# Optimization experiments

Measured on AMD Instinct MI355X. Metric: run time of the kernel, lower is better.

Reference implementation:

```python
import jax, jax.numpy as jnp
import numpy as np

SR = 22050.0  # samplerate; nyquist = SR/2


def _conv1d(x, w, b, pad):
    # x: [B, Cin, T], w: [Cout, Cin, K]
    y = jax.lax.conv_general_dilated(x, w, (1,), [(pad, pad)],
                                     dimension_numbers=('NCH', 'OIH', 'NCH'))
    return y + b[None, :, None]


def _lrelu(x):
    return jnp.where(x >= 0, x, 0.2 * x)


def _lin_upsample(x, factor):
    # torch F.upsample(mode='linear', align_corners=False) ~ half-pixel linear resize
    B, C, T = x.shape
    return jax.image.resize(x, (B, C, T * factor), method='linear')


def _oscillator_bank(f, a, sr):
    # f, a: [B, n_osc, T] -> audio [B, T]
    f = jnp.clip(f, 20.0, sr / 2.0)
    phase = jnp.cumsum(f * (2.0 * np.pi / sr), axis=-1)  # cumulative phase integration
    return jnp.sum(jnp.sin(phase) * a, axis=1)


def _noise_bank2(mags, noise):
    # mags: [B, n_coeffs, n_frames] rfft magnitudes per frame; noise: [B, total_samples]
    B, n_coeffs, n_frames = mags.shape
    window = (n_coeffs - 1) * 2
    hop = window // 2
    total = hop * n_frames
    padded = jnp.pad(noise, ((0, 0), (0, hop)))           # [B, total + hop]
    blocks = padded.reshape(B, n_frames + 1, hop)
    frames = jnp.concatenate([blocks[:, :-1], blocks[:, 1:]], axis=-1)  # [B, n_frames, window]
    spec = jnp.fft.rfft(frames, axis=-1)                   # [B, n_frames, n_coeffs]
    spec = spec * mags.transpose(0, 2, 1)                  # filter white noise per frame
    filt = jnp.fft.irfft(spec, n=window, axis=-1)          # (torch normalized rfft/irfft scales cancel)
    out = jnp.zeros((B, hop * (n_frames + 1)), filt.dtype)
    out = out.at[:, :n_frames * hop].add(filt[..., :hop].reshape(B, -1))
    out = out.at[:, hop:].add(filt[..., hop:].reshape(B, -1))
    return out[:, :total].reshape(B, 1, total)


def _forward(x, noise, mw0, mb0, mw1, mb1, mw2, mb2, mw3, mb3, fw, fb,
             gw0, gb0, gw1, gb1, gw2, gb2, gw3, gb3, lw, lb,
             nw0, nb0, nw1, nb1, nw2, nb2, nw3, nb3, nlw, nlb):
    B, _, T = x.shape
    up = noise.shape[1] // T  # upsample_factor = output_size // input_size
    n_osc = fw.shape[0]

    # oscillator frequency ranges (constants, as in __init__)
    stops = np.geomspace(20.0, SR / 2.0, num=n_osc)
    diffs = np.diff(np.concatenate([[0.0], stops]))
    starts = jnp.asarray(stops - diffs, jnp.float32)[None, :, None]
    diffs_j = jnp.asarray(diffs, jnp.float32)[None, :, None]

    # loudness path (main2 -> loudness ** 2)
    h = x
    for w_, b_ in ((gw0, gb0), (gw1, gb1), (gw2, gb2), (gw3, gb3)):
        h = _lrelu(_conv1d(h, w_, b_, 1))
    loud = _conv1d(h, lw, lb, 1) ** 2  # [B, n_osc, T]

    # frequency path (main -> sigmoid -> map to [start, stop])
    h = x
    for w_, b_ in ((mw0, mb0), (mw1, mb1), (mw2, mb2), (mw3, mb3)):
        h = _lrelu(_conv1d(h, w_, b_, 1))
    f = starts + jax.nn.sigmoid(_conv1d(h, fw, fb, 1)) * diffs_j  # [B, n_osc, T]

    h = x
    for w_, b_ in ((nw0, nb0), (nw1, nb1), (nw2, nb2), (nw3, nb3)):
        h = jnp.repeat(h, 2, axis=-1)
        h = _lrelu(_conv1d(h, w_, b_, 3))
    n_l = _conv1d(h, nlw, nlb, 1) ** 2  # [B, 17, 1024]

    loud = _lin_upsample(loud, up)  # [B, n_osc, output_size]
    f = _lin_upsample(f, up)
    harmonic = _oscillator_bank(f, loud, SR).reshape(B, 1, -1)
    return harmonic + _noise_bank2(n_l, noise)


def setup_inputs() -> dict:
    key = jax.random.key(0)
    ks = jax.random.split(key, 40)
    B, Cin, T, c, n_osc, out_size = 16, 128, 64, 512, 128, 16384
    n_coeffs = out_size // 1024 + 1  # 17
    inp = {}
    inp['x'] = jax.random.normal(ks[0], (B, Cin, T), jnp.float32)
    inp['noise'] = jax.random.uniform(ks[1], (B, out_size), jnp.float32, minval=-1.0, maxval=1.0)
    specs = [('mw0', c, Cin, 3), ('mw1', c, c, 3), ('mw2', c, c, 3), ('mw3', c, c, 3), ('fw', n_osc, c, 3),
             ('gw0', c, Cin, 3), ('gw1', c, c, 3), ('gw2', c, c, 3), ('gw3', c, c, 3), ('lw', n_osc, c, 3),
             ('nw0', c, Cin, 7), ('nw1', c, c, 7), ('nw2', c, c, 7), ('nw3', c, c, 7), ('nlw', n_coeffs, c, 3)]
    for j, (nm, o, i, ksz) in enumerate(specs):
        kw, kb = jax.random.split(ks[2 + j])
        inp[nm] = jax.random.normal(kw, (o, i, ksz), jnp.float32) * (1.0 / np.sqrt(i * ksz))
        inp[nm.replace('w', 'b', 1)] = jax.random.normal(kb, (o,), jnp.float32) * 0.01
    return inp


def reference(x, noise, mw0, mb0, mw1, mb1, mw2, mb2, mw3, mb3, fw, fb,
              gw0, gb0, gw1, gb1, gw2, gb2, gw3, gb3, lw, lb,
              nw0, nb0, nw1, nb1, nw2, nb2, nw3, nb3, nlw, nlb):
    return _forward(x, noise, mw0, mb0, mw1, mb1, mw2, mb2, mw3, mb3, fw, fb,
                    gw0, gb0, gw1, gb1, gw2, gb2, gw3, gb3, lw, lb,
                    nw0, nb0, nw1, nb1, nw2, nb2, nw3, nb3, nlw, nlb)
```

## Files before the change

kernel.cpp:

```cpp
#include <hip/hip_runtime.h>
#include <math.h>

#define ACT_LRELU  0
#define ACT_SIGMAP 1
#define ACT_SQUARE 2

typedef __attribute__((ext_vector_type(8))) short v8s;
typedef __attribute__((ext_vector_type(4))) short v4s;
typedef __attribute__((ext_vector_type(16))) float f32x16;

static __device__ __forceinline__ float lrelu(float x) { return x >= 0.f ? x : 0.2f * x; }

static __device__ __forceinline__ short bf16rne(float x) {
  unsigned u = __float_as_uint(x);
  unsigned r = (u + 0x7FFFu + ((u >> 16) & 1u)) >> 16;
  return (short)r;
}
static __device__ __forceinline__ float bf16tof(short h) {
  return __uint_as_float(((unsigned)(unsigned short)h) << 16);
}
static __device__ __forceinline__ void split3(float v, short& h, short& l, short& q) {
  h = bf16rne(v); float r1 = v - bf16tof(h);
  l = bf16rne(r1); float r2 = r1 - bf16tof(l);
  q = bf16rne(r2);
}

__global__ void __launch_bounds__(256) prep_mg(
    const float* __restrict__ x, short* __restrict__ xm3,
    const float* mw0, const float* mw1, const float* mw2, const float* mw3, const float* fw,
    const float* gw0, const float* gw1, const float* gw2, const float* gw3, const float* lw,
    short* __restrict__ mP, short* __restrict__ gP)
{
  const int blk = blockIdx.x;
  const int tid = threadIdx.x;

  if (blk < 512) {
    int e = blk * 256 + tid;
    if (e >= 131072) return;
    int b = e >> 13, rem = e & 8191, t = rem >> 7, ci = rem & 127;
    float v = x[((size_t)(b * 128) + ci) * 64 + t];
    short h, l, q; split3(v, h, l, q);
    size_t o = ((size_t)(b * 64) + t) * 128 + ci;
    xm3[0 * 131072 + o] = h;
    xm3[1 * 131072 + o] = l;
    xm3[2 * 131072 + o] = q;
    return;
  }

  int i = (blk - 512) * 256 + tid;
  const int PER = 114688;
  if (i >= 2 * PER) return;
  int path = i >= PER ? 1 : 0;
  int r = i - path * PER;
  int Cin, Cout; size_t poff;
  const float* W;
  {
    int layer;
    if (r < 8192)        { layer = 0;              Cin = 128; Cout = 512; poff = 0; }
    else if (r < 40960)  { layer = 1; r -= 8192;   Cin = 512; Cout = 512; poff = 589824; }
    else if (r < 73728)  { layer = 2; r -= 40960;  Cin = 512; Cout = 512; poff = 2949120; }
    else if (r < 106496) { layer = 3; r -= 73728;  Cin = 512; Cout = 512; poff = 5308416; }
    else                 { layer = 4; r -= 106496; Cin = 512; Cout = 128; poff = 7667712; }
    const float* Wm[5] = {mw0, mw1, mw2, mw3, fw};
    const float* Wg[5] = {gw0, gw1, gw2, gw3, lw};
    W = path ? Wg[layer] : Wm[layer];
  }
  short* P = (path ? gP : mP) + poff;
  const int nci8 = Cin >> 3;
  int co = r / nci8, ci = (r - co * nci8) * 8;
  const int K3 = 3 * Cin;
  const float* wp = W + (size_t)(co * Cin + ci) * 3;
  v8s hv[3], lv[3], qv[3];
#pragma unroll
  for (int j = 0; j < 8; ++j)
#pragma unroll
    for (int tap = 0; tap < 3; ++tap) {
      short h, l, q; split3(wp[j * 3 + tap], h, l, q);
      hv[tap][j] = h; lv[tap][j] = l; qv[tap][j] = q;
    }
#pragma unroll
  for (int tap = 0; tap < 3; ++tap) {
    size_t base = (size_t)co * K3 + tap * Cin + ci;
    *(v8s*)&P[(size_t)0 * Cout * K3 + base] = hv[tap];
    *(v8s*)&P[(size_t)1 * Cout * K3 + base] = lv[tap];
    *(v8s*)&P[(size_t)2 * Cout * K3 + base] = qv[tap];
  }
}

__global__ void __launch_bounds__(256) fold_all(
    const float* __restrict__ nw0, const float* __restrict__ nw1,
    const float* __restrict__ nw2, const float* __restrict__ nw3,
    const float* __restrict__ nlw,
    short* __restrict__ E1, short* __restrict__ E2,
    short* __restrict__ E3, short* __restrict__ E4,
    short* __restrict__ Pnl)
{
  int i = blockIdx.x * 256 + threadIdx.x;
  if (i >= 106496) {
    if (i >= 108544) return;
    int idx = i - 106496;
    int co = idx >> 6, ci = (idx & 63) * 8;
    v8s hv[3], lv[3];
#pragma unroll
    for (int j = 0; j < 8; ++j)
#pragma unroll
      for (int tap = 0; tap < 3; ++tap) {
        float v = (co < 17) ? nlw[((size_t)(co * 512 + ci + j)) * 3 + tap] : 0.f;
        short h = bf16rne(v);
        hv[tap][j] = h;
        lv[tap][j] = bf16rne(v - bf16tof(h));
      }
#pragma unroll
    for (int tap = 0; tap < 3; ++tap) {
      *(v8s*)&Pnl[(size_t)(0 * 32 + co) * 1536 + tap * 512 + ci] = hv[tap];
      *(v8s*)&Pnl[(size_t)(1 * 32 + co) * 1536 + tap * 512 + ci] = lv[tap];
    }
    return;
  }
  const float* W; short* Ag; int Cin; int idx;
  if (i < 8192)        { W = nw0; Ag = E1; Cin = 128; idx = i; }
  else if (i < 40960)  { W = nw1; Ag = E2; Cin = 512; idx = i - 8192; }
  else if (i < 73728)  { W = nw2; Ag = E3; Cin = 512; idx = i - 40960; }
  else                 { W = nw3; Ag = E4; Cin = 512; idx = i - 73728; }
  const int nci8 = Cin >> 3;
  int co = idx / nci8, ci = (idx - co * nci8) * 8;
  const float* wp = W + (size_t)(co * Cin + ci) * 7;
  const int K = Cin * 4;
  v8s he[4], le[4], ho[4], lo4[4];
#pragma unroll
  for (int j = 0; j < 8; ++j) {
    const float* w = wp + j * 7;
    float fe[4] = {w[0],        w[1] + w[2], w[3] + w[4], w[5] + w[6]};
    float fo[4] = {w[0] + w[1], w[2] + w[3], w[4] + w[5], w[6]};
#pragma unroll
    for (int q = 0; q < 4; ++q) {
      short h1 = bf16rne(fe[q]);
      he[q][j] = h1; le[q][j] = bf16rne(fe[q] - bf16tof(h1));
      short h2 = bf16rne(fo[q]);
      ho[q][j] = h2; lo4[q][j] = bf16rne(fo[q] - bf16tof(h2));
    }
  }
#pragma unroll
  for (int q = 0; q < 4; ++q) {
    size_t kbase = (size_t)q * Cin + ci;
    *(v8s*)&Ag[((size_t)(0 * 512 + co)) * K + kbase] = he[q];
    *(v8s*)&Ag[((size_t)(1 * 512 + co)) * K + kbase] = le[q];
    *(v8s*)&Ag[((size_t)(2 * 512 + co)) * K + kbase] = ho[q];
    *(v8s*)&Ag[((size_t)(3 * 512 + co)) * K + kbase] = lo4[q];
  }
}

__global__ void __launch_bounds__(256, 2) conv_path(
    const short* __restrict__ actM, const short* __restrict__ actG,
    const short* __restrict__ Pm, const short* __restrict__ Pg,
    const float* __restrict__ BsM, const float* __restrict__ BsG,
    float* __restrict__ foutM, float* __restrict__ foutG,
    short* __restrict__ soutM, short* __restrict__ soutG,
    int Cin, int Cout, int psIn, int psOut, int actMk, int actGk)
{
  const int mtiles = Cout >> 6;
  const int nblk = 2 * mtiles * 16;
  const int Q = nblk >> 3;
  int d = blockIdx.x;
  int idx = (d & 7) * Q + (d >> 3);
  int mt = idx % mtiles;
  int tmp = idx / mtiles;
  int nt = tmp & 15;
  int path = tmp >> 4;

  const short* act = path ? actG : actM;
  const short* P   = path ? Pg : Pm;
  const float* Bs  = path ? BsG : BsM;
  float* fout      = path ? foutG : foutM;
  short* sout      = path ? soutG : soutM;
  const int actk   = path ? actGk : actMk;

  const int K3 = 3 * Cin;
  const int co0 = mt * 64;
  const int n0  = nt * 64;
  const int nci = Cin >> 6;
  const int NT  = 3 * nci;

  const int tid = threadIdx.x;
  const int w = tid >> 6, wm = w & 1, wn = w >> 1;
  const int l = tid & 63;

  __shared__ __align__(16) short Al[3][64 * 72];
  __shared__ __align__(16) short Bl[3][64 * 72];
  __shared__ float bandS[2][128];

  if (actk == ACT_SIGMAP && tid < 128) {
    double lg = log(551.25);
    double stop  = 20.0 * exp(lg * (double)tid / 127.0);
    double start = (tid == 0) ? 0.0 : 20.0 * exp(lg * (double)(tid - 1) / 127.0);
    bandS[0][tid] = (float)start;
    bandS[1][tid] = (float)(stop - start);
  }

  f32x16 acc = {};
  v8s rA[3][2], rB[3][2];

  auto LOADA = [&](int t) {
    int tap = t / nci, ci0 = (t % nci) << 6;
#pragma unroll
    for (int pl = 0; pl < 3; ++pl)
#pragma unroll
      for (int it = 0; it < 2; ++it) {
        int e = it * 256 + tid;
        int row = e >> 3, c8 = e & 7;
        rA[pl][it] = *(const v8s*)&P[(size_t)pl * Cout * K3 + (size_t)(co0 + row) * K3
                                     + tap * Cin + ci0 + c8 * 8];
      }
  };
  auto LOADB = [&](int t) {
    int tap = t / nci, ci0 = (t % nci) << 6;
#pragma unroll
    for (int pl = 0; pl < 3; ++pl)
#pragma unroll
      for (int it = 0; it < 2; ++it) {
        int e = it * 256 + tid;
        int n = e >> 3, c8 = e & 7;
        int gn = n0 + n, bb = gn >> 6, trow = (gn & 63) + tap - 1;
        v8s vv = {};
        if (trow >= 0 && trow < 64)
          vv = *(const v8s*)&act[(size_t)pl * psIn + ((size_t)(bb * 64 + trow)) * Cin
                                 + ci0 + c8 * 8];
        rB[pl][it] = vv;
      }
  };
  auto WRITE = [&]() {
#pragma unroll
    for (int pl = 0; pl < 3; ++pl)
#pragma unroll
      for (int it = 0; it < 2; ++it) {
        int e = it * 256 + tid;
        int row = e >> 3, c8 = e & 7;
        *(v8s*)&Al[pl][row * 72 + c8 * 8] = rA[pl][it];
        *(v8s*)&Bl[pl][row * 72 + c8 * 8] = rB[pl][it];
      }
  };

  LOADA(0); LOADB(0);
  WRITE();
  __syncthreads();

  for (int t = 0; t < NT; ++t) {
    if (t + 1 < NT) { LOADA(t + 1); LOADB(t + 1); }
    const int abase = (wm * 32 + (l & 31)) * 72 + (l >> 5) * 8;
    const int bbase = (wn * 32 + (l & 31)) * 72 + (l >> 5) * 8;
#pragma unroll
    for (int kk = 0; kk < 4; ++kk) {
      v8s a0 = *(const v8s*)&Al[0][abase + kk * 16];
      v8s a1 = *(const v8s*)&Al[1][abase + kk * 16];
      v8s a2 = *(const v8s*)&Al[2][abase + kk * 16];
      v8s b0 = *(const v8s*)&Bl[0][bbase + kk * 16];
      v8s b1 = *(const v8s*)&Bl[1][bbase + kk * 16];
      v8s b2 = *(const v8s*)&Bl[2][bbase + kk * 16];
      acc = __builtin_amdgcn_mfma_f32_32x32x16_bf16(a0, b0, acc, 0, 0, 0);
      acc = __builtin_amdgcn_mfma_f32_32x32x16_bf16(a0, b1, acc, 0, 0, 0);
      acc = __builtin_amdgcn_mfma_f32_32x32x16_bf16(a1, b0, acc, 0, 0, 0);
      acc = __builtin_amdgcn_mfma_f32_32x32x16_bf16(a1, b1, acc, 0, 0, 0);
      acc = __builtin_amdgcn_mfma_f32_32x32x16_bf16(a0, b2, acc, 0, 0, 0);
      acc = __builtin_amdgcn_mfma_f32_32x32x16_bf16(a2, b0, acc, 0, 0, 0);
    }
    __syncthreads();
    if (t + 1 < NT) { WRITE(); __syncthreads(); }
  }

  const int ncol = wn * 32 + (l & 31);
  const int gn = n0 + ncol, bb = gn >> 6, t = gn & 63;
  const int hi4 = 4 * (l >> 5);
#pragma unroll
  for (int q4 = 0; q4 < 4; ++q4) {
    int co = co0 + wm * 32 + q4 * 8 + hi4;
    float4 bia = *(const float4*)&Bs[co];
    const float* bp = &bia.x;
    float z[4];
#pragma unroll
    for (int j = 0; j < 4; ++j) z[j] = acc[q4 * 4 + j] + bp[j];
    if (actk == ACT_LRELU) {
      v4s h4, l4, q4v;
#pragma unroll
      for (int j = 0; j < 4; ++j) {
        float zz = lrelu(z[j]);
        short h, lo, qq; split3(zz, h, lo, qq);
        h4[j] = h; l4[j] = lo; q4v[j] = qq;
      }
      size_t o = ((size_t)(bb * 64) + t) * Cout + co;
      *(v4s*)&sout[0 * (size_t)psOut + o] = h4;
      *(v4s*)&sout[1 * (size_t)psOut + o] = l4;
      *(v4s*)&sout[2 * (size_t)psOut + o] = q4v;
    } else if (actk == ACT_SIGMAP) {
#pragma unroll
      for (int j = 0; j < 4; ++j) {
        float f = bandS[0][co + j] + bandS[1][co + j] / (1.f + expf(-z[j]));
        fout[((size_t)(bb * 128) + co + j) * 64 + t] = f;
      }
    } else {
#pragma unroll
      for (int j = 0; j < 4; ++j)
        fout[((size_t)(bb * 128) + co + j) * 64 + t] = z[j] * z[j];
    }
  }
}

template<int MF, int BNS, int CIN>
__global__ void __launch_bounds__(256, 2) conv_noise(
    const short* __restrict__ actIn, const short* __restrict__ Ag,
    const float* __restrict__ Bs, short* __restrict__ actOut,
    int Sin, int psIn, int psOut)
{
  constexpr int NF   = BNS / 64;
  constexpr int BM   = MF * 64;
  constexpr int AITS = BM / 32;
  constexpr int SLAB = BNS + 3;
  constexpr int BSL  = (2 * SLAB * 8 + 255) / 256;
  constexpr int K    = CIN * 4;
  constexpr int nci  = CIN / 64;
  const int mtiles = 512 / BM;
  const int stiles = Sin / BNS;
  const int nblk = mtiles * 2 * 16 * stiles;
  const int Q = nblk >> 3;
  int d = blockIdx.x;
  int idx = (d & 7) * Q + (d >> 3);
  int mt = idx % mtiles;
  int t1 = idx / mtiles;
  int par = t1 & 1;
  int rest = t1 >> 1;
  int st = rest % stiles;
  int b = rest / stiles;

  const int co0 = mt * BM;
  const int s0 = st * BNS;
  const int soff = par ? -1 : -2;

  const int tid = threadIdx.x;
  const int w = tid >> 6, wm = w & 1, wn = w >> 1;
  const int l = tid & 63;

  __shared__ __align__(16) short Al[2][BM * 72];
  __shared__ __align__(16) short Bl[2][SLAB * 72];

  f32x16 acc[MF][NF] = {};
  v8s rA[2][AITS];
  v8s rBS[BSL];

  auto LOADA = [&](int q, int ci0) {
#pragma unroll
    for (int pl = 0; pl < 2; ++pl)
#pragma unroll
      for (int it = 0; it < AITS; ++it) {
        int e = it * 256 + tid;
        int row = e >> 3, c8 = e & 7;
        rA[pl][it] = *(const v8s*)&Ag[((size_t)((par * 2 + pl) * 512 + co0 + row)) * K
                                      + q * CIN + ci0 + c8 * 8];
      }
  };
  auto WRITEA = [&]() {
#pragma unroll
    for (int pl = 0; pl < 2; ++pl)
#pragma unroll
      for (int it = 0; it < AITS; ++it) {
        int e = it * 256 + tid;
        *(v8s*)&Al[pl][(e >> 3) * 72 + (e & 7) * 8] = rA[pl][it];
      }
  };
  auto LOADBS = [&](int ci0) {
#pragma unroll
    for (int it = 0; it < BSL; ++it) {
      int e = it * 256 + tid;
      v8s vv = {};
      if (e < 2 * SLAB * 8) {
        int r3 = e >> 3, c8 = e & 7;
        int pl = r3 / SLAB, row = r3 - pl * SLAB;
        int srow = s0 + soff + row;
        if (srow >= 0 && srow < Sin)
          vv = *(const v8s*)&actIn[(size_t)pl * psIn + ((size_t)(b * Sin + srow)) * CIN
                                   + ci0 + c8 * 8];
      }
      rBS[it] = vv;
    }
  };
  auto WRITEBS = [&]() {
#pragma unroll
    for (int it = 0; it < BSL; ++it) {
      int e = it * 256 + tid;
      if (e < 2 * SLAB * 8) {
        int r3 = e >> 3, c8 = e & 7;
        int pl = r3 / SLAB, row = r3 - pl * SLAB;
        *(v8s*)&Bl[pl][row * 72 + c8 * 8] = rBS[it];
      }
    }
  };

  LOADBS(0); LOADA(0, 0);
  WRITEBS(); WRITEA();
  __syncthreads();

  for (int ci = 0; ci < nci; ++ci) {
    const int ci0 = ci << 6;
#pragma unroll
    for (int q = 0; q < 4; ++q) {
      const bool lastq = (q == 3);
      const bool lastall = lastq && (ci == nci - 1);
      if (!lastq)        LOADA(q + 1, ci0);
      else if (!lastall) { LOADBS(ci0 + 64); LOADA(0, ci0 + 64); }

      const int lr = l & 31, lh = (l >> 5) * 8;
#pragma unroll
      for (int kk = 0; kk < 4; ++kk) {
        v8s ah[MF], al[MF], bh[NF], bl[NF];
#pragma unroll
        for (int fm = 0; fm < MF; ++fm) {
          int ab = (wm * (MF * 32) + fm * 32 + lr) * 72 + kk * 16 + lh;
          ah[fm] = *(const v8s*)&Al[0][ab];
          al[fm] = *(const v8s*)&Al[1][ab];
        }
#pragma unroll
        for (int fn = 0; fn < NF; ++fn) {
          int bb = (wn * (BNS / 2) + fn * 32 + lr + q) * 72 + kk * 16 + lh;
          bh[fn] = *(const v8s*)&Bl[0][bb];
          bl[fn] = *(const v8s*)&Bl[1][bb];
        }
#pragma unroll
        for (int fm = 0; fm < MF; ++fm)
#pragma unroll
          for (int fn = 0; fn < NF; ++fn) {
            acc[fm][fn] = __builtin_amdgcn_mfma_f32_32x32x16_bf16(ah[fm], bh[fn], acc[fm][fn], 0, 0, 0);
            acc[fm][fn] = __builtin_amdgcn_mfma_f32_32x32x16_bf16(ah[fm], bl[fn], acc[fm][fn], 0, 0, 0);
            acc[fm][fn] = __builtin_amdgcn_mfma_f32_32x32x16_bf16(al[fm], bh[fn], acc[fm][fn], 0, 0, 0);
          }
      }
      __syncthreads();
      if (!lastall) {
        if (!lastq) WRITEA();
        else { WRITEBS(); WRITEA(); }
        __syncthreads();
      }
    }
  }

  const int hi4 = 4 * (l >> 5);
  const int T2 = 2 * Sin;
#pragma unroll
  for (int fm = 0; fm < MF; ++fm)
#pragma unroll
    for (int q4 = 0; q4 < 4; ++q4) {
      int co = co0 + wm * (MF * 32) + fm * 32 + q4 * 8 + hi4;
      float4 bia = *(const float4*)&Bs[co];
      const float* bp = &bia.x;
#pragma unroll
      for (int fn = 0; fn < NF; ++fn) {
        int s_l = wn * (BNS / 2) + fn * 32 + (l & 31);
        int t = 2 * (s0 + s_l) + par;
        v4s h4, l4;
#pragma unroll
        for (int j = 0; j < 4; ++j) {
          float z = lrelu(acc[fm][fn][q4 * 4 + j] + bp[j]);
          short h = bf16rne(z);
          h4[j] = h;
          l4[j] = bf16rne(z - bf16tof(h));
        }
        size_t o = ((size_t)(b * T2) + t) * 512 + co;
        *(v4s*)&actOut[0 * (size_t)psOut + o] = h4;
        *(v4s*)&actOut[1 * (size_t)psOut + o] = l4;
      }
    }
}

#define NL_PS4 8388608

__global__ void __launch_bounds__(128) conv_nl_filter(
    const short* __restrict__ act, const short* __restrict__ Pnl,
    const float* __restrict__ Bs, const float* __restrict__ noise,
    float* __restrict__ filt)
{
  const int bid = blockIdx.x;
  const int b = bid >> 4, t0 = (bid & 15) << 6;
  const int tid = threadIdx.x;
  const int w = tid >> 6;
  const int l = tid & 63;

  __shared__ __align__(16) short Al[2 * 3 * 32 * 72];
  __shared__ __align__(16) short Bl[2 * 66 * 72];
  __shared__ float magS[64][20];
  __shared__ float ctS[32], stS[32];

  if (tid < 32) {
    double a = (double)tid * (3.14159265358979323846 / 16.0);
    ctS[tid] = (float)cos(a);
    stS[tid] = (float)sin(a);
  }

  f32x16 acc = {};

  for (int ci0 = 0; ci0 < 512; ci0 += 64) {
    for (int e = tid; e < 1536; e += 128) {
      int c8 = e & 7, row = e >> 3;
      int pl = row >= 96;
      int r2 = row - pl * 96;
      int tap = r2 >> 5, co = r2 & 31;
      v8s vv = *(const v8s*)&Pnl[(size_t)(pl * 32 + co) * 1536 + tap * 512 + ci0 + c8 * 8];
      *(v8s*)&Al[row * 72 + c8 * 8] = vv;
    }
    for (int e = tid; e < 1056; e += 128) {
      int c8 = e & 7, r = (e >> 3) % 66, pl = (e >> 3) / 66;
      int t = t0 + r - 1;
      v8s vv = {};
      if (t >= 0 && t < 1024)
        vv = *(const v8s*)&act[(size_t)pl * NL_PS4 + ((size_t)(b << 10) + t) * 512 + ci0 + c8 * 8];
      *(v8s*)&Bl[(pl * 66 + r) * 72 + c8 * 8] = vv;
    }
    __syncthreads();
    const int lr = l & 31, lh = (l >> 5) * 8;
#pragma unroll
    for (int kk = 0; kk < 4; ++kk)
#pragma unroll
      for (int tap = 0; tap < 3; ++tap) {
        v8s a_h = *(const v8s*)&Al[((0 * 3 + tap) * 32 + lr) * 72 + kk * 16 + lh];
        v8s a_l = *(const v8s*)&Al[((1 * 3 + tap) * 32 + lr) * 72 + kk * 16 + lh];
        int brow = w * 32 + lr + tap;
        v8s b_h = *(const v8s*)&Bl[(0 * 66 + brow) * 72 + kk * 16 + lh];
        v8s b_l = *(const v8s*)&Bl[(1 * 66 + brow) * 72 + kk * 16 + lh];
        acc = __builtin_amdgcn_mfma_f32_32x32x16_bf16(a_h, b_h, acc, 0, 0, 0);
        acc = __builtin_amdgcn_mfma_f32_32x32x16_bf16(a_h, b_l, acc, 0, 0, 0);
        acc = __builtin_amdgcn_mfma_f32_32x32x16_bf16(a_l, b_h, acc, 0, 0, 0);
      }
    __syncthreads();
  }

  const int t_loc = w * 32 + (l & 31);
  const int hi4 = 4 * (l >> 5);
#pragma unroll
  for (int q4 = 0; q4 < 4; ++q4)
#pragma unroll
    for (int j = 0; j < 4; ++j) {
      int co = q4 * 8 + hi4 + j;
      if (co < 17) {
        float z = acc[q4 * 4 + j] + Bs[co];
        magS[t_loc][co] = z * z;
      }
    }
  __syncthreads();

  if (tid < 64) {
    int i = t0 + tid;
    float xv[32];
#pragma unroll
    for (int n = 0; n < 32; ++n) {
      int idx = i * 16 + n;
      xv[n] = (idx < 16384) ? noise[(size_t)b * 16384 + idx] : 0.f;
    }
    float Yr[17], Yi[17];
#pragma unroll
    for (int k = 0; k <= 16; ++k) {
      float xr = 0.f, xi = 0.f;
      int kk = 0;
#pragma unroll
      for (int n = 0; n < 32; ++n) {
        xr += xv[n] * ctS[kk];
        xi -= xv[n] * stS[kk];
        kk = (kk + k) & 31;
      }
      float m = magS[tid][k];
      Yr[k] = xr * m;
      Yi[k] = xi * m;
    }
    float* fo = filt + ((size_t)(b << 10) + i) * 32;
#pragma unroll
    for (int n = 0; n < 32; ++n) {
      float v = Yr[0] + ((n & 1) ? -Yr[16] : Yr[16]);
      int kk = n;
#pragma unroll
      for (int k = 1; k <= 15; ++k) {
        v += 2.f * (Yr[k] * ctS[kk] - Yi[k] * stS[kk]);
        kk = (kk + n) & 31;
      }
      fo[n] = v * (1.f / 32.f);
    }
  }
}

static __device__ __forceinline__ int clamp64(int i) { return i < 0 ? 0 : (i > 63 ? 63 : i); }

__global__ void __launch_bounds__(256) osc_phase(
    const float* __restrict__ fsm, double* __restrict__ phaseBase)
{
  const int o = blockIdx.x, b = blockIdx.y;
  const float* frow = fsm + (size_t)(b * 128 + o) * 64;
  const int c = threadIdx.x;

  const float ic0 = ((float)(c * 64) - 127.5f) * (1.0f / 256.0f);
  const int ilo = (int)floorf(ic0);
  float f0 = frow[clamp64(ilo)], f1 = frow[clamp64(ilo + 1)], f2 = frow[clamp64(ilo + 2)];

  double local = 0.0;
#pragma unroll 8
  for (int j = 0; j < 64; ++j) {
    float ic = ic0 + (float)j * (1.0f / 256.0f);
    float fl = floorf(ic);
    float w  = ic - fl;
    bool hi = ((int)fl) > ilo;
    float fa = hi ? f1 : f0;
    float fb = hi ? f2 : f1;
    float f = fa * (1.f - w) + fb * w;
    f = fminf(fmaxf(f, 20.f), 11025.f);
    local += (double)f;
  }
  local *= (1.0 / 22050.0);

  __shared__ double ps[256];
  ps[c] = local;
  __syncthreads();
  for (int off = 1; off < 256; off <<= 1) {
    double v = (c >= off) ? ps[c - off] : 0.0;
    __syncthreads();
    ps[c] += v;
    __syncthreads();
  }
  phaseBase[(size_t)(b * 128 + o) * 256 + c] = ps[c] - local;
}

__global__ void __launch_bounds__(128) osc_sum(
    const float* __restrict__ fsm, const float* __restrict__ lsm,
    const double* __restrict__ phaseBase, const float* __restrict__ filt,
    float* __restrict__ out)
{
  const int c = blockIdx.x, b = blockIdx.y;
  const int tid = threadIdx.x;
  __shared__ float contrib[128][65];
  __shared__ float part[2][64];
  const int o = tid;
  const float* frow = fsm + (size_t)(b * 128 + o) * 64;
  const float* arow = lsm + (size_t)(b * 128 + o) * 64;

  double pb = phaseBase[(size_t)(b * 128 + o) * 256 + c];
  float fb0 = (float)(pb - floor(pb));

  const float ic0 = ((float)(c * 64) - 127.5f) * (1.0f / 256.0f);
  const int ilo = (int)floorf(ic0);
  float f0 = frow[clamp64(ilo)], f1 = frow[clamp64(ilo + 1)], f2 = frow[clamp64(ilo + 2)];
  float a0 = arow[clamp64(ilo)], a1 = arow[clamp64(ilo + 1)], a2 = arow[clamp64(ilo + 2)];

  float rel = 0.f, comp = 0.f;
#pragma unroll 8
  for (int j = 0; j < 64; ++j) {
    float ic = ic0 + (float)j * (1.0f / 256.0f);
    float fl = floorf(ic);
    float w  = ic - fl;
    bool hi = ((int)fl) > ilo;
    float fa = hi ? f1 : f0;
    float fb = hi ? f2 : f1;
    float f = fa * (1.f - w) + fb * w;
    f = fminf(fmaxf(f, 20.f), 11025.f);
    float y = f * (1.0f / 22050.0f) - comp;
    float t = rel + y;
    comp = (t - rel) - y;
    rel = t;
    float tot = fb0 + rel;
    float frac = tot - floorf(tot);
    float s = sinpif(2.f * frac);
    float aa = hi ? a1 : a0;
    float ab = hi ? a2 : a1;
    float am = aa * (1.f - w) + ab * w;
    contrib[o][j] = s * am;
  }
  __syncthreads();
  int half = tid >> 6, tl = tid & 63;
  float sum = 0.f;
  for (int oo = 0; oo < 64; ++oo) sum += contrib[half * 64 + oo][tl];
  part[half][tl] = sum;
  __syncthreads();
  if (tid < 64) {
    int t = c * 64 + tid;
    float v = part[0][tid] + part[1][tid];
    int i0 = t >> 4, r = t & 15;
    v += filt[((size_t)(b << 10) + i0) * 32 + r];
    if (i0 > 0) v += filt[((size_t)(b << 10) + i0 - 1) * 32 + 16 + r];
    out[(size_t)b * 16384 + t] = v;
  }
}

extern "C" void kernel_launch(void* const* d_in, const int* in_sizes, int n_in,
                              void* d_out, int out_size, void* d_ws, size_t ws_size,
                              hipStream_t stream)
{
  (void)in_sizes; (void)n_in; (void)out_size; (void)ws_size;

  const float* x     = (const float*)d_in[0];
  const float* noise = (const float*)d_in[1];
  const float* mw0 = (const float*)d_in[2];  const float* mb0 = (const float*)d_in[3];
  const float* mw1 = (const float*)d_in[4];  const float* mb1 = (const float*)d_in[5];
  const float* mw2 = (const float*)d_in[6];  const float* mb2 = (const float*)d_in[7];
  const float* mw3 = (const float*)d_in[8];  const float* mb3 = (const float*)d_in[9];
  const float* fw  = (const float*)d_in[10]; const float* fb  = (const float*)d_in[11];
  const float* gw0 = (const float*)d_in[12]; const float* gb0 = (const float*)d_in[13];
  const float* gw1 = (const float*)d_in[14]; const float* gb1 = (const float*)d_in[15];
  const float* gw2 = (const float*)d_in[16]; const float* gb2 = (const float*)d_in[17];
  const float* gw3 = (const float*)d_in[18]; const float* gb3 = (const float*)d_in[19];
  const float* lw  = (const float*)d_in[20]; const float* lb  = (const float*)d_in[21];
  const float* nw0 = (const float*)d_in[22]; const float* nb0 = (const float*)d_in[23];
  const float* nw1 = (const float*)d_in[24]; const float* nb1 = (const float*)d_in[25];
  const float* nw2 = (const float*)d_in[26]; const float* nb2 = (const float*)d_in[27];
  const float* nw3 = (const float*)d_in[28]; const float* nb3 = (const float*)d_in[29];
  const float* nlw = (const float*)d_in[30]; const float* nlb = (const float*)d_in[31];

  char* W8 = (char*)d_ws;
  short* mP  = (short*)(W8 + 0);
  short* gP  = (short*)(W8 + 16515072);
  short* hm0 = (short*)(W8 + 33030144);
  short* hm1 = (short*)(W8 + 36175872);
  short* hg0 = (short*)(W8 + 39321600);
  short* hg1 = (short*)(W8 + 42467328);
  short* xm3 = (short*)(W8 + 58720256);
  float* fsm = (float*)(W8 + 59506688);
  float* lsm = (float*)(W8 + 60030976);
  short* Pnl = (short*)(W8 + 60555264);

  short* E4  = (short*)(W8 + 0);
  short* E3  = (short*)(W8 + 33554432);
  short* E2  = (short*)(W8 + 41943040);
  short* E1  = (short*)(W8 + 50331648);
  short* l1out = (short*)(W8 + 52428800);
  short* l2out = (short*)(W8 + 25165824);
  short* l3out = (short*)(W8 + 8388608);
  short* l4act = (short*)(W8 + 25165824);

  float* filt = (float*)(W8 + 1114112);
  double* phaseBase = (double*)(W8 + 4194304);

  float* out = (float*)d_out;

  const int PS_X = 131072;
  const int PS_H = 524288;

  prep_mg<<<1408, 256, 0, stream>>>(x, xm3,
      mw0, mw1, mw2, mw3, fw, gw0, gw1, gw2, gw3, lw, mP, gP);

  conv_path<<<256, 256, 0, stream>>>(xm3, xm3, mP + 0, gP + 0, mb0, gb0,
      nullptr, nullptr, hm0, hg0, 128, 512, PS_X, PS_H, ACT_LRELU, ACT_LRELU);
  conv_path<<<256, 256, 0, stream>>>(hm0, hg0, mP + 589824, gP + 589824, mb1, gb1,
      nullptr, nullptr, hm1, hg1, 512, 512, PS_H, PS_H, ACT_LRELU, ACT_LRELU);
  conv_path<<<256, 256, 0, stream>>>(hm1, hg1, mP + 2949120, gP + 2949120, mb2, gb2,
      nullptr, nullptr, hm0, hg0, 512, 512, PS_H, PS_H, ACT_LRELU, ACT_LRELU);
  conv_path<<<256, 256, 0, stream>>>(hm0, hg0, mP + 5308416, gP + 5308416, mb3, gb3,
      nullptr, nullptr, hm1, hg1, 512, 512, PS_H, PS_H, ACT_LRELU, ACT_LRELU);
  conv_path<<<64, 256, 0, stream>>>(hm1, hg1, mP + 7667712, gP + 7667712, fb, lb,
      fsm, lsm, nullptr, nullptr, 512, 128, PS_H, 0, ACT_SIGMAP, ACT_SQUARE);

  fold_all<<<424, 256, 0, stream>>>(nw0, nw1, nw2, nw3, nlw, E1, E2, E3, E4, Pnl);
  conv_noise<1, 64, 128><<<256, 256, 0, stream>>>(xm3, E1, nb0, l1out, 64, PS_X, 1048576);
  conv_noise<2, 64, 512><<<256, 256, 0, stream>>>(l1out, E2, nb1, l2out, 128, 1048576, 2097152);
  conv_noise<2, 128, 512><<<256, 256, 0, stream>>>(l2out, E3, nb2, l3out, 256, 2097152, 4194304);
  conv_noise<2, 128, 512><<<512, 256, 0, stream>>>(l3out, E4, nb3, l4act, 512, 4194304, 8388608);

  conv_nl_filter<<<256, 128, 0, stream>>>(l4act, Pnl, nlb, noise, filt);

  osc_phase<<<dim3(128, 16), 256, 0, stream>>>(fsm, phaseBase);
  osc_sum<<<dim3(256, 16), 128, 0, stream>>>(fsm, lsm, phaseBase, filt, out);
}
```

Before: 507.7 us.

## Co-schedule harmonic and noise conv layers in fused launches with separate workspace

When the workspace is large enough, the two independent conv chains share launches. Each fused launch runs the mel/gain path conv blocks and the noise-path conv blocks side by side, using a shared-memory union. The weight prep and fold kernels are merged into one launch. This needs non-aliased buffers, so a new workspace layout is used, and the old aliased schedule is kept as a fallback. The aim is to cut launch count and fill idle CUs in each layer, at the cost of larger shared memory per block and possible uneven block durations.

```diff
diff --git a/kernel.cpp b/kernel.cpp
--- a/kernel.cpp
+++ b/kernel.cpp
@@ -25,11 +25,33 @@
   q = bf16rne(r2);
 }
 
-__global__ void __launch_bounds__(256) prep_mg(
+struct SMPathT {
+  short Al[3][64 * 72];
+  short Bl[3][64 * 72];
+  float bandS[2][128];
+};
+template<int BM, int SLAB>
+struct SMNoiseT {
+  short Al[2][BM * 72];
+  short Bl[2][SLAB * 72];
+};
+template<int BM, int SLAB>
+union SMFusedU {
+  SMPathT p;
+  SMNoiseT<BM, SLAB> n;
+};
+
+__global__ void __launch_bounds__(256) prep_all(
     const float* __restrict__ x, short* __restrict__ xm3,
     const float* mw0, const float* mw1, const float* mw2, const float* mw3, const float* fw,
     const float* gw0, const float* gw1, const float* gw2, const float* gw3, const float* lw,
-    short* __restrict__ mP, short* __restrict__ gP)
+    short* __restrict__ mP, short* __restrict__ gP,
+    const float* __restrict__ nw0, const float* __restrict__ nw1,
+    const float* __restrict__ nw2, const float* __restrict__ nw3,
+    const float* __restrict__ nlw,
+    short* __restrict__ E1, short* __restrict__ E2,
+    short* __restrict__ E3, short* __restrict__ E4,
+    short* __restrict__ Pnl)
 {
   const int blk = blockIdx.x;
   const int tid = threadIdx.x;
@@ -47,55 +69,49 @@
     return;
   }
 
-  int i = (blk - 512) * 256 + tid;
-  const int PER = 114688;
-  if (i >= 2 * PER) return;
-  int path = i >= PER ? 1 : 0;
-  int r = i - path * PER;
-  int Cin, Cout; size_t poff;
-  const float* W;
-  {
-    int layer;
-    if (r < 8192)        { layer = 0;              Cin = 128; Cout = 512; poff = 0; }
-    else if (r < 40960)  { layer = 1; r -= 8192;   Cin = 512; Cout = 512; poff = 589824; }
-    else if (r < 73728)  { layer = 2; r -= 40960;  Cin = 512; Cout = 512; poff = 2949120; }
-    else if (r < 106496) { layer = 3; r -= 73728;  Cin = 512; Cout = 512; poff = 5308416; }
-    else                 { layer = 4; r -= 106496; Cin = 512; Cout = 128; poff = 7667712; }
-    const float* Wm[5] = {mw0, mw1, mw2, mw3, fw};
-    const float* Wg[5] = {gw0, gw1, gw2, gw3, lw};
-    W = path ? Wg[layer] : Wm[layer];
-  }
-  short* P = (path ? gP : mP) + poff;
-  const int nci8 = Cin >> 3;
-  int co = r / nci8, ci = (r - co * nci8) * 8;
-  const int K3 = 3 * Cin;
-  const float* wp = W + (size_t)(co * Cin + ci) * 3;
-  v8s hv[3], lv[3], qv[3];
-#pragma unroll
-  for (int j = 0; j < 8; ++j)
+  if (blk < 1408) {
+    int i = (blk - 512) * 256 + tid;
+    const int PER = 114688;
+    if (i >= 2 * PER) return;
+    int path = i >= PER ? 1 : 0;
+    int r = i - path * PER;
+    int Cin, Cout; size_t poff;
+    const float* W;
+    {
+      int layer;
+      if (r < 8192)        { layer = 0;              Cin = 128; Cout = 512; poff = 0; }
+      else if (r < 40960)  { layer = 1; r -= 8192;   Cin = 512; Cout = 512; poff = 589824; }
+      else if (r < 73728)  { layer = 2; r -= 40960;  Cin = 512; Cout = 512; poff = 2949120; }
+      else if (r < 106496) { layer = 3; r -= 73728;  Cin = 512; Cout = 512; poff = 5308416; }
+      else                 { layer = 4; r -= 106496; Cin = 512; Cout = 128; poff = 7667712; }
+      const float* Wm[5] = {mw0, mw1, mw2, mw3, fw};
+      const float* Wg[5] = {gw0, gw1, gw2, gw3, lw};
+      W = path ? Wg[layer] : Wm[layer];
+    }
+    short* P = (path ? gP : mP) + poff;
+    const int nci8 = Cin >> 3;
+    int co = r / nci8, ci = (r - co * nci8) * 8;
+    const int K3 = 3 * Cin;
+    const float* wp = W + (size_t)(co * Cin + ci) * 3;
+    v8s hv[3], lv[3], qv[3];
+#pragma unroll
+    for (int j = 0; j < 8; ++j)
+#pragma unroll
+      for (int tap = 0; tap < 3; ++tap) {
+        short h, l, q; split3(wp[j * 3 + tap], h, l, q);
+        hv[tap][j] = h; lv[tap][j] = l; qv[tap][j] = q;
+      }
 #pragma unroll
     for (int tap = 0; tap < 3; ++tap) {
-      short h, l, q; split3(wp[j * 3 + tap], h, l, q);
-      hv[tap][j] = h; lv[tap][j] = l; qv[tap][j] = q;
-    }
-#pragma unroll
-  for (int tap = 0; tap < 3; ++tap) {
-    size_t base = (size_t)co * K3 + tap * Cin + ci;
-    *(v8s*)&P[(size_t)0 * Cout * K3 + base] = hv[tap];
-    *(v8s*)&P[(size_t)1 * Cout * K3 + base] = lv[tap];
-    *(v8s*)&P[(size_t)2 * Cout * K3 + base] = qv[tap];
-  }
-}
-
-__global__ void __launch_bounds__(256) fold_all(
-    const float* __restrict__ nw0, const float* __restrict__ nw1,
-    const float* __restrict__ nw2, const float* __restrict__ nw3,
-    const float* __restrict__ nlw,
-    short* __restrict__ E1, short* __restrict__ E2,
-    short* __restrict__ E3, short* __restrict__ E4,
-    short* __restrict__ Pnl)
-{
-  int i = blockIdx.x * 256 + threadIdx.x;
+      size_t base = (size_t)co * K3 + tap * Cin + ci;
+      *(v8s*)&P[(size_t)0 * Cout * K3 + base] = hv[tap];
+      *(v8s*)&P[(size_t)1 * Cout * K3 + base] = lv[tap];
+      *(v8s*)&P[(size_t)2 * Cout * K3 + base] = qv[tap];
+    }
+    return;
+  }
+
+  int i = (blk - 1408) * 256 + tid;
   if (i >= 106496) {
     if (i >= 108544) return;
     int idx = i - 106496;
@@ -150,7 +166,8 @@
   }
 }
 
-__global__ void __launch_bounds__(256, 2) conv_path(
+__device__ __forceinline__ void conv_path_body(
+    SMPathT& sm, int bidx,
     const short* __restrict__ actM, const short* __restrict__ actG,
     const short* __restrict__ Pm, const short* __restrict__ Pg,
     const float* __restrict__ BsM, const float* __restrict__ BsG,
@@ -161,7 +178,7 @@
   const int mtiles = Cout >> 6;
   const int nblk = 2 * mtiles * 16;
   const int Q = nblk >> 3;
-  int d = blockIdx.x;
+  int d = bidx;
   int idx = (d & 7) * Q + (d >> 3);
   int mt = idx % mtiles;
   int tmp = idx / mtiles;
@@ -185,16 +202,12 @@
   const int w = tid >> 6, wm = w & 1, wn = w >> 1;
   const int l = tid & 63;
 
-  __shared__ __align__(16) short Al[3][64 * 72];
-  __shared__ __align__(16) short Bl[3][64 * 72];
-  __shared__ float bandS[2][128];
-
   if (actk == ACT_SIGMAP && tid < 128) {
     double lg = log(551.25);
     double stop  = 20.0 * exp(lg * (double)tid / 127.0);
     double start = (tid == 0) ? 0.0 : 20.0 * exp(lg * (double)(tid - 1) / 127.0);
-    bandS[0][tid] = (float)start;
-    bandS[1][tid] = (float)(stop - start);
+    sm.bandS[0][tid] = (float)start;
+    sm.bandS[1][tid] = (float)(stop - start);
   }
 
   f32x16 acc = {};
@@ -235,8 +248,8 @@
       for (int it = 0; it < 2; ++it) {
         int e = it * 256 + tid;
         int row = e >> 3, c8 = e & 7;
-        *(v8s*)&Al[pl][row * 72 + c8 * 8] = rA[pl][it];
-        *(v8s*)&Bl[pl][row * 72 + c8 * 8] = rB[pl][it];
+        *(v8s*)&sm.Al[pl][row * 72 + c8 * 8] = rA[pl][it];
+        *(v8s*)&sm.Bl[pl][row * 72 + c8 * 8] = rB[pl][it];
       }
   };
 
@@ -250,12 +263,12 @@
     const int bbase = (wn * 32 + (l & 31)) * 72 + (l >> 5) * 8;
 #pragma unroll
     for (int kk = 0; kk < 4; ++kk) {
-      v8s a0 = *(const v8s*)&Al[0][abase + kk * 16];
-      v8s a1 = *(const v8s*)&Al[1][abase + kk * 16];
-      v8s a2 = *(const v8s*)&Al[2][abase + kk * 16];
-      v8s b0 = *(const v8s*)&Bl[0][bbase + kk * 16];
-      v8s b1 = *(const v8s*)&Bl[1][bbase + kk * 16];
-      v8s b2 = *(const v8s*)&Bl[2][bbase + kk * 16];
+      v8s a0 = *(const v8s*)&sm.Al[0][abase + kk * 16];
+      v8s a1 = *(const v8s*)&sm.Al[1][abase + kk * 16];
+      v8s a2 = *(const v8s*)&sm.Al[2][abase + kk * 16];
+      v8s b0 = *(const v8s*)&sm.Bl[0][bbase + kk * 16];
+      v8s b1 = *(const v8s*)&sm.Bl[1][bbase + kk * 16];
+      v8s b2 = *(const v8s*)&sm.Bl[2][bbase + kk * 16];
       acc = __builtin_amdgcn_mfma_f32_32x32x16_bf16(a0, b0, acc, 0, 0, 0);
       acc = __builtin_amdgcn_mfma_f32_32x32x16_bf16(a0, b1, acc, 0, 0, 0);
       acc = __builtin_amdgcn_mfma_f32_32x32x16_bf16(a1, b0, acc, 0, 0, 0);
@@ -293,7 +306,7 @@
     } else if (actk == ACT_SIGMAP) {
 #pragma unroll
       for (int j = 0; j < 4; ++j) {
-        float f = bandS[0][co + j] + bandS[1][co + j] / (1.f + expf(-z[j]));
+        float f = sm.bandS[0][co + j] + sm.bandS[1][co + j] / (1.f + expf(-z[j]));
         fout[((size_t)(bb * 128) + co + j) * 64 + t] = f;
       }
     } else {
@@ -305,7 +318,8 @@
 }
 
 template<int MF, int BNS, int CIN>
-__global__ void __launch_bounds__(256, 2) conv_noise(
+__device__ __forceinline__ void conv_noise_body(
+    SMNoiseT<MF * 64, BNS + 3>& sm, int bidx,
     const short* __restrict__ actIn, const short* __restrict__ Ag,
     const float* __restrict__ Bs, short* __restrict__ actOut,
     int Sin, int psIn, int psOut)
@@ -321,7 +335,7 @@
   const int stiles = Sin / BNS;
   const int nblk = mtiles * 2 * 16 * stiles;
   const int Q = nblk >> 3;
-  int d = blockIdx.x;
+  int d = bidx;
   int idx = (d & 7) * Q + (d >> 3);
   int mt = idx % mtiles;
   int t1 = idx / mtiles;
@@ -338,9 +352,6 @@
   const int w = tid >> 6, wm = w & 1, wn = w >> 1;
   const int l = tid & 63;
 
-  __shared__ __align__(16) short Al[2][BM * 72];
-  __shared__ __align__(16) short Bl[2][SLAB * 72];
-
   f32x16 acc[MF][NF] = {};
   v8s rA[2][AITS];
   v8s rBS[BSL];
@@ -362,7 +373,7 @@
 #pragma unroll
       for (int it = 0; it < AITS; ++it) {
         int e = it * 256 + tid;
-        *(v8s*)&Al[pl][(e >> 3) * 72 + (e & 7) * 8] = rA[pl][it];
+        *(v8s*)&sm.Al[pl][(e >> 3) * 72 + (e & 7) * 8] = rA[pl][it];
       }
   };
   auto LOADBS = [&](int ci0) {
@@ -388,7 +399,7 @@
       if (e < 2 * SLAB * 8) {
         int r3 = e >> 3, c8 = e & 7;
         int pl = r3 / SLAB, row = r3 - pl * SLAB;
-        *(v8s*)&Bl[pl][row * 72 + c8 * 8] = rBS[it];
+        *(v8s*)&sm.Bl[pl][row * 72 + c8 * 8] = rBS[it];
       }
     }
   };
@@ -413,14 +424,14 @@
 #pragma unroll
         for (int fm = 0; fm < MF; ++fm) {
           int ab = (wm * (MF * 32) + fm * 32 + lr) * 72 + kk * 16 + lh;
-          ah[fm] = *(const v8s*)&Al[0][ab];
-          al[fm] = *(const v8s*)&Al[1][ab];
+          ah[fm] = *(const v8s*)&sm.Al[0][ab];
+          al[fm] = *(const v8s*)&sm.Al[1][ab];
         }
 #pragma unroll
         for (int fn = 0; fn < NF; ++fn) {
           int bb = (wn * (BNS / 2) + fn * 32 + lr + q) * 72 + kk * 16 + lh;
-          bh[fn] = *(const v8s*)&Bl[0][bb];
-          bl[fn] = *(const v8s*)&Bl[1][bb];
+          bh[fn] = *(const v8s*)&sm.Bl[0][bb];
+          bl[fn] = *(const v8s*)&sm.Bl[1][bb];
         }
 #pragma unroll
         for (int fm = 0; fm < MF; ++fm)
@@ -466,6 +477,107 @@
         *(v4s*)&actOut[1 * (size_t)psOut + o] = l4;
       }
     }
+}
+
+__global__ void __launch_bounds__(256, 2) k_conv_path(
+    const short* actM, const short* actG, const short* Pm, const short* Pg,
+    const float* BsM, const float* BsG,
+    float* foutM, float* foutG, short* soutM, short* soutG,
+    int Cin, int Cout, int psIn, int psOut, int actMk, int actGk)
+{
+  __shared__ SMPathT sm;
+  conv_path_body(sm, blockIdx.x, actM, actG, Pm, Pg, BsM, BsG,
+                 foutM, foutG, soutM, soutG, Cin, Cout, psIn, psOut, actMk, actGk);
+}
+
+template<int MF, int BNS, int CIN>
+__global__ void __launch_bounds__(256, 2) k_conv_noise(
+    const short* actIn, const short* Ag, const float* Bs, short* actOut,
+    int Sin, int psIn, int psOut)
+{
+  __shared__ SMNoiseT<MF * 64, BNS + 3> sm;
+  conv_noise_body<MF, BNS, CIN>(sm, blockIdx.x, actIn, Ag, Bs, actOut, Sin, psIn, psOut);
+}
+
+template<int MF, int BNS, int CIN>
+__global__ void __launch_bounds__(256, 2) k_fused(
+    const short* actM, const short* actG, const short* Pm, const short* Pg,
+    const float* BsM, const float* BsG,
+    float* foutM, float* foutG, short* soutM, short* soutG,
+    int Cin, int Cout, int psIn, int psOut, int actMk, int actGk,
+    const short* nActIn, const short* nAg, const float* nBs, short* nActOut,
+    int nSin, int nPsIn, int nPsOut, int mgBlocks)
+{
+  __shared__ SMFusedU<MF * 64, BNS + 3> sm;
+  if ((int)blockIdx.x < mgBlocks)
+    conv_path_body(sm.p, blockIdx.x, actM, actG, Pm, Pg, BsM, BsG,
+                   foutM, foutG, soutM, soutG, Cin, Cout, psIn, psOut, actMk, actGk);
+  else
+    conv_noise_body<MF, BNS, CIN>(sm.n, blockIdx.x - mgBlocks,
+                                  nActIn, nAg, nBs, nActOut, nSin, nPsIn, nPsOut);
+}
+
+__global__ void __launch_bounds__(256) fold_all(
+    const float* __restrict__ nw0, const float* __restrict__ nw1,
+    const float* __restrict__ nw2, const float* __restrict__ nw3,
+    const float* __restrict__ nlw,
+    short* __restrict__ E1, short* __restrict__ E2,
+    short* __restrict__ E3, short* __restrict__ E4,
+    short* __restrict__ Pnl)
+{
+  int i = blockIdx.x * 256 + threadIdx.x;
+  if (i >= 106496) {
+    if (i >= 108544) return;
+    int idx = i - 106496;
+    int co = idx >> 6, ci = (idx & 63) * 8;
+    v8s hv[3], lv[3];
+#pragma unroll
+    for (int j = 0; j < 8; ++j)
+#pragma unroll
+      for (int tap = 0; tap < 3; ++tap) {
+        float v = (co < 17) ? nlw[((size_t)(co * 512 + ci + j)) * 3 + tap] : 0.f;
+        short h = bf16rne(v);
+        hv[tap][j] = h;
+        lv[tap][j] = bf16rne(v - bf16tof(h));
+      }
+#pragma unroll
+    for (int tap = 0; tap < 3; ++tap) {
+      *(v8s*)&Pnl[(size_t)(0 * 32 + co) * 1536 + tap * 512 + ci] = hv[tap];
+      *(v8s*)&Pnl[(size_t)(1 * 32 + co) * 1536 + tap * 512 + ci] = lv[tap];
+    }
+    return;
+  }
+  const float* W; short* Ag; int Cin; int idx;
+  if (i < 8192)        { W = nw0; Ag = E1; Cin = 128; idx = i; }
+  else if (i < 40960)  { W = nw1; Ag = E2; Cin = 512; idx = i - 8192; }
+  else if (i < 73728)  { W = nw2; Ag = E3; Cin = 512; idx = i - 40960; }
+  else                 { W = nw3; Ag = E4; Cin = 512; idx = i - 73728; }
+  const int nci8 = Cin >> 3;
+  int co = idx / nci8, ci = (idx - co * nci8) * 8;
+  const float* wp = W + (size_t)(co * Cin + ci) * 7;
+  const int K = Cin * 4;
+  v8s he[4], le[4], ho[4], lo4[4];
+#pragma unroll
+  for (int j = 0; j < 8; ++j) {
+    const float* w = wp + j * 7;
+    float fe[4] = {w[0],        w[1] + w[2], w[3] + w[4], w[5] + w[6]};
+    float fo[4] = {w[0] + w[1], w[2] + w[3], w[4] + w[5], w[6]};
+#pragma unroll
+    for (int q = 0; q < 4; ++q) {
+      short h1 = bf16rne(fe[q]);
+      he[q][j] = h1; le[q][j] = bf16rne(fe[q] - bf16tof(h1));
+      short h2 = bf16rne(fo[q]);
+      ho[q][j] = h2; lo4[q][j] = bf16rne(fo[q] - bf16tof(h2));
+    }
+  }
+#pragma unroll
+  for (int q = 0; q < 4; ++q) {
+    size_t kbase = (size_t)q * Cin + ci;
+    *(v8s*)&Ag[((size_t)(0 * 512 + co)) * K + kbase] = he[q];
+    *(v8s*)&Ag[((size_t)(1 * 512 + co)) * K + kbase] = le[q];
+    *(v8s*)&Ag[((size_t)(2 * 512 + co)) * K + kbase] = ho[q];
+    *(v8s*)&Ag[((size_t)(3 * 512 + co)) * K + kbase] = lo4[q];
+  }
 }
 
 #define NL_PS4 8388608
@@ -685,7 +797,7 @@
                               void* d_out, int out_size, void* d_ws, size_t ws_size,
                               hipStream_t stream)
 {
-  (void)in_sizes; (void)n_in; (void)out_size; (void)ws_size;
+  (void)in_sizes; (void)n_in; (void)out_size;
 
   const float* x     = (const float*)d_in[0];
   const float* noise = (const float*)d_in[1];
@@ -706,56 +818,108 @@
   const float* nlw = (const float*)d_in[30]; const float* nlb = (const float*)d_in[31];
 
   char* W8 = (char*)d_ws;
-  short* mP  = (short*)(W8 + 0);
-  short* gP  = (short*)(W8 + 16515072);
-  short* hm0 = (short*)(W8 + 33030144);
-  short* hm1 = (short*)(W8 + 36175872);
-  short* hg0 = (short*)(W8 + 39321600);
-  short* hg1 = (short*)(W8 + 42467328);
-  short* xm3 = (short*)(W8 + 58720256);
-  float* fsm = (float*)(W8 + 59506688);
-  float* lsm = (float*)(W8 + 60030976);
-  short* Pnl = (short*)(W8 + 60555264);
-
-  short* E4  = (short*)(W8 + 0);
-  short* E3  = (short*)(W8 + 33554432);
-  short* E2  = (short*)(W8 + 41943040);
-  short* E1  = (short*)(W8 + 50331648);
-  short* l1out = (short*)(W8 + 52428800);
-  short* l2out = (short*)(W8 + 25165824);
-  short* l3out = (short*)(W8 + 8388608);
-  short* l4act = (short*)(W8 + 25165824);
-
-  float* filt = (float*)(W8 + 1114112);
-  double* phaseBase = (double*)(W8 + 4194304);
-
   float* out = (float*)d_out;
-
   const int PS_X = 131072;
   const int PS_H = 524288;
 
-  prep_mg<<<1408, 256, 0, stream>>>(x, xm3,
-      mw0, mw1, mw2, mw3, fw, gw0, gw1, gw2, gw3, lw, mP, gP);
-
-  conv_path<<<256, 256, 0, stream>>>(xm3, xm3, mP + 0, gP + 0, mb0, gb0,
-      nullptr, nullptr, hm0, hg0, 128, 512, PS_X, PS_H, ACT_LRELU, ACT_LRELU);
-  conv_path<<<256, 256, 0, stream>>>(hm0, hg0, mP + 589824, gP + 589824, mb1, gb1,
-      nullptr, nullptr, hm1, hg1, 512, 512, PS_H, PS_H, ACT_LRELU, ACT_LRELU);
-  conv_path<<<256, 256, 0, stream>>>(hm1, hg1, mP + 2949120, gP + 2949120, mb2, gb2,
-      nullptr, nullptr, hm0, hg0, 512, 512, PS_H, PS_H, ACT_LRELU, ACT_LRELU);
-  conv_path<<<256, 256, 0, stream>>>(hm0, hg0, mP + 5308416, gP + 5308416, mb3, gb3,
-      nullptr, nullptr, hm1, hg1, 512, 512, PS_H, PS_H, ACT_LRELU, ACT_LRELU);
-  conv_path<<<64, 256, 0, stream>>>(hm1, hg1, mP + 7667712, gP + 7667712, fb, lb,
-      fsm, lsm, nullptr, nullptr, 512, 128, PS_H, 0, ACT_SIGMAP, ACT_SQUARE);
-
-  fold_all<<<424, 256, 0, stream>>>(nw0, nw1, nw2, nw3, nlw, E1, E2, E3, E4, Pnl);
-  conv_noise<1, 64, 128><<<256, 256, 0, stream>>>(xm3, E1, nb0, l1out, 64, PS_X, 1048576);
-  conv_noise<2, 64, 512><<<256, 256, 0, stream>>>(l1out, E2, nb1, l2out, 128, 1048576, 2097152);
-  conv_noise<2, 128, 512><<<256, 256, 0, stream>>>(l2out, E3, nb2, l3out, 256, 2097152, 4194304);
-  conv_noise<2, 128, 512><<<512, 256, 0, stream>>>(l3out, E4, nb3, l4act, 512, 4194304, 8388608);
-
-  conv_nl_filter<<<256, 128, 0, stream>>>(l4act, Pnl, nlb, noise, filt);
-
-  osc_phase<<<dim3(128, 16), 256, 0, stream>>>(fsm, phaseBase);
-  osc_sum<<<dim3(256, 16), 128, 0, stream>>>(fsm, lsm, phaseBase, filt, out);
-}
+  const bool bigws = (ws_size >= 144113664ull);
+
+  if (bigws) {
+    short* mP  = (short*)(W8 + 0);
+    short* gP  = (short*)(W8 + 16515072);
+    short* hm0 = (short*)(W8 + 33030144);
+    short* hm1 = (short*)(W8 + 36175872);
+    short* hg0 = (short*)(W8 + 39321600);
+    short* hg1 = (short*)(W8 + 42467328);
+    short* xm3 = (short*)(W8 + 45613056);
+    float* fsm = (float*)(W8 + 46399488);
+    float* lsm = (float*)(W8 + 46923776);
+    short* Pnl = (short*)(W8 + 47448064);
+    short* E1  = (short*)(W8 + 47644672);
+    short* E2  = (short*)(W8 + 49741824);
+    short* E3  = (short*)(W8 + 58130432);
+    short* E4  = (short*)(W8 + 66519040);
+    short* l1out = (short*)(W8 + 74907648);
+    short* l2out = (short*)(W8 + 79101952);
+    short* l3out = (short*)(W8 + 87490560);
+    short* l4act = (short*)(W8 + 104267776);
+    float* filt  = (float*)(W8 + 137822208);
+    double* phaseBase = (double*)(W8 + 139919360);
+
+    prep_all<<<1832, 256, 0, stream>>>(x, xm3,
+        mw0, mw1, mw2, mw3, fw, gw0, gw1, gw2, gw3, lw, mP, gP,
+        nw0, nw1, nw2, nw3, nlw, E1, E2, E3, E4, Pnl);
+
+    k_fused<1, 64, 128><<<512, 256, 0, stream>>>(
+        xm3, xm3, mP + 0, gP + 0, mb0, gb0, nullptr, nullptr, hm0, hg0,
+        128, 512, PS_X, PS_H, ACT_LRELU, ACT_LRELU,
+        xm3, E1, nb0, l1out, 64, PS_X, 1048576, 256);
+    k_fused<2, 64, 512><<<512, 256, 0, stream>>>(
+        hm0, hg0, mP + 589824, gP + 589824, mb1, gb1, nullptr, nullptr, hm1, hg1,
+        512, 512, PS_H, PS_H, ACT_LRELU, ACT_LRELU,
+        l1out, E2, nb1, l2out, 128, 1048576, 2097152, 256);
+    k_fused<2, 128, 512><<<512, 256, 0, stream>>>(
+        hm1, hg1, mP + 2949120, gP + 2949120, mb2, gb2, nullptr, nullptr, hm0, hg0,
+        512, 512, PS_H, PS_H, ACT_LRELU, ACT_LRELU,
+        l2out, E3, nb2, l3out, 256, 2097152, 4194304, 256);
+    k_fused<2, 128, 512><<<768, 256, 0, stream>>>(
+        hm0, hg0, mP + 5308416, gP + 5308416, mb3, gb3, nullptr, nullptr, hm1, hg1,
+        512, 512, PS_H, PS_H, ACT_LRELU, ACT_LRELU,
+        l3out, E4, nb3, l4act, 512, 4194304, 8388608, 256);
+
+    k_conv_path<<<64, 256, 0, stream>>>(hm1, hg1, mP + 7667712, gP + 7667712, fb, lb,
+        fsm, lsm, nullptr, nullptr, 512, 128, PS_H, 0, ACT_SIGMAP, ACT_SQUARE);
+
+    conv_nl_filter<<<256, 128, 0, stream>>>(l4act, Pnl, nlb, noise, filt);
+    osc_phase<<<dim3(128, 16), 256, 0, stream>>>(fsm, phaseBase);
+    osc_sum<<<dim3(256, 16), 128, 0, stream>>>(fsm, lsm, phaseBase, filt, out);
+  } else {
+    short* mP  = (short*)(W8 + 0);
+    short* gP  = (short*)(W8 + 16515072);
+    short* hm0 = (short*)(W8 + 33030144);
+    short* hm1 = (short*)(W8 + 36175872);
+    short* hg0 = (short*)(W8 + 39321600);
+    short* hg1 = (short*)(W8 + 42467328);
+    short* xm3 = (short*)(W8 + 58720256);
+    float* fsm = (float*)(W8 + 59506688);
+    float* lsm = (float*)(W8 + 60030976);
+    short* Pnl = (short*)(W8 + 60555264);
+
+    short* E4  = (short*)(W8 + 0);
+    short* E3  = (short*)(W8 + 33554432);
+    short* E2  = (short*)(W8 + 41943040);
+    short* E1  = (short*)(W8 + 50331648);
+    short* l1out = (short*)(W8 + 52428800);
+    short* l2out = (short*)(W8 + 25165824);
+    short* l3out = (short*)(W8 + 8388608);
+    short* l4act = (short*)(W8 + 25165824);
+
+    float* filt = (float*)(W8 + 1114112);
+    double* phaseBase = (double*)(W8 + 4194304);
+
+    prep_all<<<1408, 256, 0, stream>>>(x, xm3,
+        mw0, mw1, mw2, mw3, fw, gw0, gw1, gw2, gw3, lw, mP, gP,
+        nw0, nw1, nw2, nw3, nlw, E1, E2, E3, E4, Pnl);
+
+    k_conv_path<<<256, 256, 0, stream>>>(xm3, xm3, mP + 0, gP + 0, mb0, gb0,
+        nullptr, nullptr, hm0, hg0, 128, 512, PS_X, PS_H, ACT_LRELU, ACT_LRELU);
+    k_conv_path<<<256, 256, 0, stream>>>(hm0, hg0, mP + 589824, gP + 589824, mb1, gb1,
+        nullptr, nullptr, hm1, hg1, 512, 512, PS_H, PS_H, ACT_LRELU, ACT_LRELU);
+    k_conv_path<<<256, 256, 0, stream>>>(hm1, hg1, mP + 2949120, gP + 2949120, mb2, gb2,
+        nullptr, nullptr, hm0, hg0, 512, 512, PS_H, PS_H, ACT_LRELU, ACT_LRELU);
+    k_conv_path<<<256, 256, 0, stream>>>(hm0, hg0, mP + 5308416, gP + 5308416, mb3, gb3,
+        nullptr, nullptr, hm1, hg1, 512, 512, PS_H, PS_H, ACT_LRELU, ACT_LRELU);
+    k_conv_path<<<64, 256, 0, stream>>>(hm1, hg1, mP + 7667712, gP + 7667712, fb, lb,
+        fsm, lsm, nullptr, nullptr, 512, 128, PS_H, 0, ACT_SIGMAP, ACT_SQUARE);
+
+    fold_all<<<424, 256, 0, stream>>>(nw0, nw1, nw2, nw3, nlw, E1, E2, E3, E4, Pnl);
+    k_conv_noise<1, 64, 128><<<256, 256, 0, stream>>>(xm3, E1, nb0, l1out, 64, PS_X, 1048576);
+    k_conv_noise<2, 64, 512><<<256, 256, 0, stream>>>(l1out, E2, nb1, l2out, 128, 1048576, 2097152);
+    k_conv_noise<2, 128, 512><<<256, 256, 0, stream>>>(l2out, E3, nb2, l3out, 256, 2097152, 4194304);
+    k_conv_noise<2, 128, 512><<<512, 256, 0, stream>>>(l3out, E4, nb3, l4act, 512, 4194304, 8388608);
+
+    conv_nl_filter<<<256, 128, 0, stream>>>(l4act, Pnl, nlb, noise, filt);
+    osc_phase<<<dim3(128, 16), 256, 0, stream>>>(fsm, phaseBase);
+    osc_sum<<<dim3(256, 16), 128, 0, stream>>>(fsm, lsm, phaseBase, filt, out);
+  }
+}
```

After: 721.0 us. 1.42x slower.
